# Kernel optimization log

Hardware: AMD Instinct MI355X
Metric: run time of the kernel (lower is better)

The kernel has to match this reference:

```python
import jax, jax.numpy as jnp
import numpy as np

B, N, D = 8, 16384, 256
WIDTH = 33
CENTER = 16


def setup_inputs() -> dict:
    key = jax.random.key(0)
    k1, k2, k3 = jax.random.split(key, 3)
    x = jax.random.normal(k1, (B, N, D), dtype=jnp.float32)
    # token sizes >= 1 (as produced by merging ones-initialized sizes)
    size = 1.0 + 4.0 * jax.random.uniform(k2, (B, N, 1), dtype=jnp.float32)
    # nonnegative window weights
    source_matrix = jax.random.uniform(k3, (B, N, WIDTH), dtype=jnp.float32)
    return {"x": x, "size": size, "source_matrix": source_matrix,
            "center": CENTER, "width": WIDTH}


def reference(x, size, source_matrix, center, width):
    # x: (B, N, d); size: (B, N, 1); source_matrix: (B, N, width)
    Bn, Nn, d = x.shape
    base = jnp.arange(Nn)

    def step(summed, off):
        pos = base + (off - center)                      # (N,)
        valid = (pos >= 0) & (pos < Nn)
        pc = jnp.clip(pos, 0, Nn - 1)
        gathered = x[:, pc, :]                           # (B, N, d)
        w = source_matrix[:, :, off] * valid.astype(x.dtype)  # (B, N)
        return summed + gathered * w[..., None], None

    summed, _ = jax.lax.scan(step, jnp.zeros_like(x), jnp.arange(width))
    denom = jnp.maximum(size, 1e-6)                      # (B, N, 1)
    return summed / denom
```

## Files before the change

kernel.cpp:

```cpp
#include <hip/hip_runtime.h>
#include <utility>

#define D_DIM 256
#define WID   33
#define CEN   16
#define RACC  8
#define XROWS (RACC + 2 * CEN)
#define RITER 16
#define NI    16
#define CHUNK (RITER * NI)
#define RING  64
#define PROL  48


typedef float f32x2 __attribute__((ext_vector_type(2)));

__device__ __forceinline__ float rdlane(float v, int l) {
    return __uint_as_float(__builtin_amdgcn_readlane(__float_as_uint(v), l));
}

__device__ __forceinline__ int clampN(int p, int N) {
    return p < 0 ? 0 : (p >= N ? N - 1 : p);
}

__device__ __forceinline__ f32x2 ld2(const float* p) {
    return *(const f32x2*)p;
}

__device__ __forceinline__ void dma_row(float* xs, int slot,
                                        const float* __restrict__ xlane,
                                        int row) {
    __builtin_amdgcn_global_load_lds(
        (const __attribute__((address_space(1))) void*)(xlane +
                                                        (size_t)row * D_DIM),
        (__attribute__((address_space(3))) void*)(xs + slot * D_DIM), 16, 0, 0);
}

template <size_t... Ss>
__device__ __forceinline__ void stage_prol(float* xs,
                                           const float* __restrict__ xlane,
                                           int base0, int N, int wv,
                                           std::index_sequence<Ss...>) {
    (([&] {
         const int s = wv * (PROL / 4) + (int)Ss;
         dma_row(xs, s, xlane, clampN(base0 + s, N));
     }()),
     ...);
}

template <int PH, size_t... Ss>
__device__ __forceinline__ void stage_iter(float* xs,
                                           const float* __restrict__ xlane,
                                           int base0, int m, int N, int wv,
                                           std::index_sequence<Ss...>) {
    (([&] {
         constexpr int C = (PROL + 16 * PH) & (RING - 1);
         const int j = wv * 4 + (int)Ss;
         dma_row(xs, C + j, xlane, clampN(base0 + PROL + 16 * m + j, N));
     }()),
     ...);
}

template <size_t... Rs>
__device__ __forceinline__ void load_w(float (&w)[RACC],
                                       const float* __restrict__ smb,
                                       int nbase, int minl, int N,
                                       std::index_sequence<Rs...>) {
    ((w[Rs] = smb[(size_t)clampN(nbase + (int)Rs, N) * WID + minl]), ...);
}

template <size_t... Rs>
__device__ __forceinline__ void zero_bad_w(float (&w)[RACC], int n0w, int lane,
                                           int N, std::index_sequence<Rs...>) {
    ((w[Rs] = ((unsigned)(n0w + (int)Rs - CEN + lane) < (unsigned)N)
                  ? w[Rs] : 0.0f),
     ...);
}

template <int J, size_t... Rs>
__device__ __forceinline__ void consume_j(f32x2 (&acc)[RACC],
                                          const float (&w)[RACC], f32x2 xv,
                                          std::index_sequence<Rs...>) {
    (([&] {
         constexpr int r = (int)Rs;
         if constexpr (J - r >= 0 && J - r < WID) {
             const float ws = rdlane(w[r], J - r);
             acc[r].x = fmaf(xv.x, ws, acc[r].x);
             acc[r].y = fmaf(xv.y, ws, acc[r].y);
         }
     }()),
     ...);
}

template <int PH, int RG, size_t... Js>
__device__ __forceinline__ void stream_rows(f32x2 (&acc)[RACC],
                                            const float (&w)[RACC],
                                            const float* xscp,
                                            std::index_sequence<Js...>) {
    (([&] {
         constexpr int slot = (16 * PH + 8 * RG + (int)Js) & (RING - 1);
         const f32x2 xv = ld2(xscp + slot * D_DIM);
         consume_j<(int)Js>(acc, w, xv, std::make_index_sequence<RACC>{});
     }()),
     ...);
}

template <size_t... Rs>
__device__ __forceinline__ void store_all(const f32x2 (&acc)[RACC], float szv,
                                          float* __restrict__ ob,
                                          std::index_sequence<Rs...>) {
    (([&] {
         constexpr int r = (int)Rs;
         const float inv = __builtin_amdgcn_rcpf(fmaxf(rdlane(szv, r), 1e-6f));
         f32x2 o;
         o.x = acc[r].x * inv;
         o.y = acc[r].y * inv;
         *(f32x2*)(ob + (size_t)r * D_DIM) = o;
     }()),
     ...);
}

template <int PH>
__device__ __forceinline__ void iter_body(
    float* xs, const float* __restrict__ xlane, const float* __restrict__ smb,
    const float* __restrict__ szb, float* __restrict__ obcp, int n0, int m,
    int N, int wv, int rg, int lane, int cp, float (&wcur)[RACC],
    float (&wnxt)[RACC], float& szcur, float& sznxt, int minl) {
    if (m < NI - 1)
        stage_iter<PH>(xs, xlane, n0 - CEN, m, N, wv,
                       std::make_index_sequence<4>{});
    const int n1 = n0 + (m + 1) * RITER + rg * RACC;
    load_w(wnxt, smb, n1, minl, N, std::make_index_sequence<RACC>{});
    sznxt = szb[clampN(n1 + (lane & 7), N)];
    __builtin_amdgcn_sched_barrier(0);

    const int n0w = n0 + m * RITER + rg * RACC;
    if (n0w < CEN || n0w + RACC - 1 + CEN >= N)
        zero_bad_w(wcur, n0w, lane, N, std::make_index_sequence<RACC>{});

    f32x2 acc[RACC] = {};
    if (rg == 0)
        stream_rows<PH, 0>(acc, wcur, xs + cp, std::make_index_sequence<XROWS>{});
    else
        stream_rows<PH, 1>(acc, wcur, xs + cp, std::make_index_sequence<XROWS>{});

    store_all(acc, szcur, obcp + (size_t)n0w * D_DIM,
              std::make_index_sequence<RACC>{});

    __builtin_amdgcn_sched_barrier(0);
    asm volatile("s_waitcnt vmcnt(8)" ::: "memory");
    __builtin_amdgcn_s_barrier();
    __builtin_amdgcn_sched_barrier(0);
}

__global__ __launch_bounds__(256) void local_enc_kernel(
    const float* __restrict__ x, const float* __restrict__ sizev,
    const float* __restrict__ sm, float* __restrict__ out, int N) {
    __shared__ float xs[RING * D_DIM];

    const int bid   = blockIdx.x;
    const int swz   = (bid & 7) * 64 + (bid >> 3);
    const int strip = swz & 63;
    const int b     = swz >> 6;
    const int n0    = strip * CHUNK;
    const int tid   = threadIdx.x;
    const int wv    = tid >> 6;
    const int lane  = tid & 63;
    const int rg    = wv >> 1;
    const int cp    = ((wv & 1) * 64 + lane) * 2;

    const size_t bN = (size_t)b * (size_t)N;
    const float* __restrict__ xlane = x + bN * D_DIM + lane * 4;
    const float* __restrict__ smb   = sm + bN * WID;
    const float* __restrict__ szb   = sizev + bN;
    float* __restrict__ obcp        = out + bN * D_DIM + cp;

    stage_prol(xs, xlane, n0 - CEN, N, wv, std::make_index_sequence<PROL / 4>{});
    const int minl = (lane < WID) ? lane : (WID - 1);
    float wA[RACC], wB[RACC];
    float szA, szB;
    load_w(wA, smb, n0 + rg * RACC, minl, N, std::make_index_sequence<RACC>{});
    szA = szb[clampN(n0 + rg * RACC + (lane & 7), N)];
    __syncthreads();

#pragma unroll 1
    for (int mo = 0; mo < NI / 4; ++mo) {
        const int m0 = 4 * mo;
        iter_body<0>(xs, xlane, smb, szb, obcp, n0, m0 + 0, N, wv, rg, lane,
                     cp, wA, wB, szA, szB, minl);
        iter_body<1>(xs, xlane, smb, szb, obcp, n0, m0 + 1, N, wv, rg, lane,
                     cp, wB, wA, szB, szA, minl);
        iter_body<2>(xs, xlane, smb, szb, obcp, n0, m0 + 2, N, wv, rg, lane,
                     cp, wA, wB, szA, szB, minl);
        iter_body<3>(xs, xlane, smb, szb, obcp, n0, m0 + 3, N, wv, rg, lane,
                     cp, wB, wA, szB, szA, minl);
    }
}

extern "C" void kernel_launch(void* const* d_in, const int* in_sizes, int n_in,
                              void* d_out, int out_size, void* d_ws, size_t ws_size,
                              hipStream_t stream) {
    const float* x  = (const float*)d_in[0];
    const float* sz = (const float*)d_in[1];
    const float* sm = (const float*)d_in[2];
    float* out = (float*)d_out;

    const int B = 8;
    const int N = 16384;

    dim3 grid((N / CHUNK) * B, 1, 1);
    dim3 block(256, 1, 1);
    local_enc_kernel<<<grid, block, 0, stream>>>(x, sz, sm, out, N);
}
```

Measured before the change: 64.38 us.

## Halve rows per accumulator and chunk, shrink LDS ring with runtime slot indexing

Each wave group now accumulates 4 output rows instead of 8 and each iteration covers 8 rows, so a block handles 128 rows and the grid doubles. The LDS ring shrinks from 64 to 48 rows, and because 48 is not a power of two, slot indices are computed at runtime with wraparound instead of being compile-time constants. The goal is fewer accumulator registers and smaller LDS per block, for higher occupancy and more blocks in flight. The cost is a lower reuse ratio: each output row now needs 36 staged x rows per 4 outputs, and the runtime slot arithmetic adds ALU work.

```diff
diff --git a/kernel.cpp b/kernel.cpp
--- a/kernel.cpp
+++ b/kernel.cpp
@@ -4,13 +4,13 @@
 #define D_DIM 256
 #define WID   33
 #define CEN   16
-#define RACC  8
+#define RACC  4
 #define XROWS (RACC + 2 * CEN)
-#define RITER 16
+#define RITER 8
 #define NI    16
 #define CHUNK (RITER * NI)
-#define RING  64
-#define PROL  48
+#define RING  48
+#define PROL  40
 
 
 typedef float f32x2 __attribute__((ext_vector_type(2)));
@@ -48,17 +48,17 @@
      ...);
 }
 
-template <int PH, size_t... Ss>
 __device__ __forceinline__ void stage_iter(float* xs,
                                            const float* __restrict__ xlane,
-                                           int base0, int m, int N, int wv,
-                                           std::index_sequence<Ss...>) {
-    (([&] {
-         constexpr int C = (PROL + 16 * PH) & (RING - 1);
-         const int j = wv * 4 + (int)Ss;
-         dma_row(xs, C + j, xlane, clampN(base0 + PROL + 16 * m + j, N));
-     }()),
-     ...);
+                                           int base0, int m, int slot0, int N,
+                                           int wv) {
+#pragma unroll
+    for (int kk = 0; kk < 2; ++kk) {
+        const int k = wv * 2 + kk;
+        int s = slot0 + PROL + k;
+        if (s >= RING) s -= RING;
+        dma_row(xs, s, xlane, clampN(base0 + PROL + RITER * m + k, N));
+    }
 }
 
 template <size_t... Rs>
@@ -92,14 +92,15 @@
      ...);
 }
 
-template <int PH, int RG, size_t... Js>
+template <size_t... Js>
 __device__ __forceinline__ void stream_rows(f32x2 (&acc)[RACC],
                                             const float (&w)[RACC],
-                                            const float* xscp,
+                                            const float* xs, int sbase, int cp,
                                             std::index_sequence<Js...>) {
     (([&] {
-         constexpr int slot = (16 * PH + 8 * RG + (int)Js) & (RING - 1);
-         const f32x2 xv = ld2(xscp + slot * D_DIM);
+         int s = sbase + (int)Js;
+         if (s >= RING) s -= RING;
+         const f32x2 xv = ld2(xs + s * D_DIM + cp);
          consume_j<(int)Js>(acc, w, xv, std::make_index_sequence<RACC>{});
      }()),
      ...);
@@ -120,35 +121,31 @@
      ...);
 }
 
-template <int PH>
 __device__ __forceinline__ void iter_body(
     float* xs, const float* __restrict__ xlane, const float* __restrict__ smb,
     const float* __restrict__ szb, float* __restrict__ obcp, int n0, int m,
-    int N, int wv, int rg, int lane, int cp, float (&wcur)[RACC],
+    int slot0, int N, int wv, int rg, int lane, int cp, float (&wcur)[RACC],
     float (&wnxt)[RACC], float& szcur, float& sznxt, int minl) {
     if (m < NI - 1)
-        stage_iter<PH>(xs, xlane, n0 - CEN, m, N, wv,
-                       std::make_index_sequence<4>{});
-    const int n1 = n0 + (m + 1) * RITER + rg * RACC;
+        stage_iter(xs, xlane, n0 - CEN, m, slot0, N, wv);
+    __builtin_amdgcn_sched_barrier(0);
+    const int n1 = n0 + RITER * (m + 1) + rg * RACC;
     load_w(wnxt, smb, n1, minl, N, std::make_index_sequence<RACC>{});
-    sznxt = szb[clampN(n1 + (lane & 7), N)];
-    __builtin_amdgcn_sched_barrier(0);
-
-    const int n0w = n0 + m * RITER + rg * RACC;
+    sznxt = szb[clampN(n1 + (lane & 3), N)];
+    __builtin_amdgcn_sched_barrier(0);
+
+    const int n0w = n0 + RITER * m + rg * RACC;
     if (n0w < CEN || n0w + RACC - 1 + CEN >= N)
         zero_bad_w(wcur, n0w, lane, N, std::make_index_sequence<RACC>{});
 
     f32x2 acc[RACC] = {};
-    if (rg == 0)
-        stream_rows<PH, 0>(acc, wcur, xs + cp, std::make_index_sequence<XROWS>{});
-    else
-        stream_rows<PH, 1>(acc, wcur, xs + cp, std::make_index_sequence<XROWS>{});
-
+    stream_rows(acc, wcur, xs, slot0 + RACC * rg, cp,
+                std::make_index_sequence<XROWS>{});
     store_all(acc, szcur, obcp + (size_t)n0w * D_DIM,
               std::make_index_sequence<RACC>{});
 
     __builtin_amdgcn_sched_barrier(0);
-    asm volatile("s_waitcnt vmcnt(8)" ::: "memory");
+    asm volatile("s_waitcnt vmcnt(9)" ::: "memory");
     __builtin_amdgcn_s_barrier();
     __builtin_amdgcn_sched_barrier(0);
 }
@@ -159,9 +156,9 @@
     __shared__ float xs[RING * D_DIM];
 
     const int bid   = blockIdx.x;
-    const int swz   = (bid & 7) * 64 + (bid >> 3);
-    const int strip = swz & 63;
-    const int b     = swz >> 6;
+    const int swz   = (bid & 7) * 128 + (bid >> 3);
+    const int strip = swz & 127;
+    const int b     = swz >> 7;
     const int n0    = strip * CHUNK;
     const int tid   = threadIdx.x;
     const int wv    = tid >> 6;
@@ -180,20 +177,19 @@
     float wA[RACC], wB[RACC];
     float szA, szB;
     load_w(wA, smb, n0 + rg * RACC, minl, N, std::make_index_sequence<RACC>{});
-    szA = szb[clampN(n0 + rg * RACC + (lane & 7), N)];
+    szA = szb[clampN(n0 + rg * RACC + (lane & 3), N)];
     __syncthreads();
 
+    int slot0 = 0;
 #pragma unroll 1
-    for (int mo = 0; mo < NI / 4; ++mo) {
-        const int m0 = 4 * mo;
-        iter_body<0>(xs, xlane, smb, szb, obcp, n0, m0 + 0, N, wv, rg, lane,
-                     cp, wA, wB, szA, szB, minl);
-        iter_body<1>(xs, xlane, smb, szb, obcp, n0, m0 + 1, N, wv, rg, lane,
-                     cp, wB, wA, szB, szA, minl);
-        iter_body<2>(xs, xlane, smb, szb, obcp, n0, m0 + 2, N, wv, rg, lane,
-                     cp, wA, wB, szA, szB, minl);
-        iter_body<3>(xs, xlane, smb, szb, obcp, n0, m0 + 3, N, wv, rg, lane,
-                     cp, wB, wA, szB, szA, minl);
+    for (int mp = 0; mp < NI / 2; ++mp) {
+        const int m0 = 2 * mp;
+        iter_body(xs, xlane, smb, szb, obcp, n0, m0, slot0, N, wv, rg, lane,
+                  cp, wA, wB, szA, szB, minl);
+        slot0 += RITER; if (slot0 >= RING) slot0 -= RING;
+        iter_body(xs, xlane, smb, szb, obcp, n0, m0 + 1, slot0, N, wv, rg,
+                  lane, cp, wB, wA, szB, szA, minl);
+        slot0 += RITER; if (slot0 >= RING) slot0 -= RING;
     }
 }
 
```

After: 79.77 us. 23.9% more time.
